# Optimization experiments

Hardware: AMD Instinct MI355X
Metric: run time of the kernel (lower is better)

## Reference

```python
import jax, jax.numpy as jnp
import numpy as np

V = 5000      # vocab_size
N = 10000     # num_training_size
T = 50        # num_topics
H = 200       # en_units
B = 1024      # batch
K = 20        # num_k
ALPHA = 1.0
ETA = 0.5
RHO = 0.5
EPS = 1e-5    # BatchNorm eps
CC = 0.25     # TopicDistQuant commitment cost


def _xavier(key, shape):
    fan_out, fan_in = shape
    lim = float(np.sqrt(6.0 / (fan_in + fan_out)))
    return jax.random.uniform(key, shape, jnp.float32, -lim, lim)


def setup_inputs() -> dict:
    key = jax.random.key(0)
    ks = jax.random.split(key, 10)
    return {
        'idx': jax.random.randint(ks[0], (B,), 0, N),
        'inputs': jax.random.uniform(ks[1], (B, V), jnp.float32),
        'is_aug': 1,
        'training_data': jax.random.uniform(ks[2], (N, V), jnp.float32),
        'M_cos_dist': jax.random.uniform(ks[3], (N, N), jnp.float32),
        'M_coo_dist': jax.random.uniform(ks[4], (N, N), jnp.float32),
        'theta_bank': jax.random.uniform(ks[5], (N, T), jnp.float32),
        'W11': _xavier(ks[6], (H, V)), 'b11': jnp.zeros((H,), jnp.float32),
        'W12': _xavier(ks[7], (H, H)), 'b12': jnp.zeros((H,), jnp.float32),
        'W21': _xavier(ks[8], (T, H)), 'b21': jnp.zeros((T,), jnp.float32),
        'g_mean': jnp.ones((T,), jnp.float32), 'beta_mean': jnp.zeros((T,), jnp.float32),
        'g_dec': jnp.ones((V,), jnp.float32), 'beta_dec': jnp.zeros((V,), jnp.float32),
        'Wd': _xavier(ks[9], (V, T)),
        'E': jnp.eye(T, dtype=jnp.float32),  # TopicDistQuant codebook (identity init)
    }


def _batchnorm(x, g, b):
    # training-mode BatchNorm1d: batch mean, biased variance
    m = x.mean(axis=0)
    v = x.var(axis=0)
    return (x - m) / jnp.sqrt(v + EPS) * g + b


def _forward(idx, inputs, is_aug, training_data, M_cos_dist, M_coo_dist, theta_bank,
             W11, b11, W12, b12, W21, b21, g_mean, beta_mean, g_dec, beta_dec, Wd, E):
    # encoder
    e1 = jax.nn.softplus(inputs @ W11.T + b11)          # [B,H]
    e1 = jax.nn.softplus(e1 @ W12.T + b12)              # [B,H]
    theta = _batchnorm(e1 @ W21.T + b21, g_mean, beta_mean)  # [B,T]
    softmax_theta = jax.nn.softmax(theta, axis=1)

    # TopicDistQuant (VQ with straight-through, identity codebook)
    d = ((softmax_theta ** 2).sum(1, keepdims=True)
         + (E ** 2).sum(1) - 2.0 * softmax_theta @ E.T)  # [B,T]
    enc_idx = jnp.argmin(d, axis=1)                      # [B]
    quantized = E[enc_idx]                               # [B,T]
    e_latent = jnp.mean((jax.lax.stop_gradient(quantized) - softmax_theta) ** 2)
    q_latent = jnp.mean((quantized - jax.lax.stop_gradient(softmax_theta)) ** 2)
    quant_loss = q_latent + CC * e_latent
    quant = softmax_theta + jax.lax.stop_gradient(quantized - softmax_theta)

    # decoder
    recon = jax.nn.softmax(_batchnorm(quant @ Wd.T, g_dec, beta_dec), axis=1)  # [B,V]

    if is_aug:
        # get_aug_x: fused distance + topk + gather-sum over training bank
        td = jax.lax.stop_gradient(softmax_theta)        # theta.detach()
        cost = ((td ** 2).sum(1, keepdims=True)
                + (theta_bank ** 2).sum(1) - 2.0 * td @ theta_bank.T)  # [B,N]
        theta_dist = jnp.square(cost)                    # torch.square(cost)
        bow_dist = RHO * M_cos_dist[idx] + (1.0 - RHO) * M_coo_dist[idx]  # [B,N]
        fuse = ETA * theta_dist + (1.0 - ETA) * bow_dist
        fuse = fuse.at[jnp.arange(B), idx].set(jnp.inf)  # mask self
        _, topk_idx = jax.lax.top_k(-fuse, K)            # K smallest -> [B,K]
        aug_x = (ALPHA / K) * jnp.take(training_data, topk_idx, axis=0).sum(axis=1)  # [B,V]
        x = inputs + aug_x
    else:
        x = inputs

    rec_loss = jnp.mean(-(x * jnp.log(recon)).sum(axis=1))
    return rec_loss + quant_loss


def reference(idx, inputs, is_aug, training_data, M_cos_dist, M_coo_dist, theta_bank,
              W11, b11, W12, b12, W21, b21, g_mean, beta_mean, g_dec, beta_dec, Wd, E):
    return _forward(idx, inputs, is_aug, training_data, M_cos_dist, M_coo_dist, theta_bank,
                    W11, b11, W12, b12, W21, b21, g_mean, beta_mean, g_dec, beta_dec, Wd, E)
```

## Files before the change

kernel.cpp:

```cpp
#include <hip/hip_runtime.h>
#include <math.h>

#define B_ 1024
#define V_ 5000
#define N_ 10000
#define T_ 50
#define H_ 200
#define K_ 20
#define EPS_ 1e-5f

__device__ __forceinline__ float sp_(float x) {
    return (x > 20.f) ? x : log1pf(expf(x));
}

__global__ __launch_bounds__(256) void k_init(float* e1a, float* buckets, int* cnt) {
    int i = blockIdx.x * 256 + threadIdx.x;
    if (i < B_ * H_) e1a[i] = 0.f;
    if (i < 1024)    buckets[i] = 0.f;
    if (i < 64)      cnt[i] = 0;
}

__global__ __launch_bounds__(256) void k_gemm1(const float* __restrict__ X,
                                               const float* __restrict__ W,
                                               float* __restrict__ e1a) {
    __shared__ __align__(16) float Al[64][8];
    __shared__ __align__(16) float Bl[200][8];
    const int tid = threadIdx.x;
    const int r = tid & 31, c = tid >> 5;
    const int m0 = blockIdx.x * 64;
    const int k0 = blockIdx.y * 200;
    float acc0[25], acc1[25];
#pragma unroll
    for (int j = 0; j < 25; ++j) { acc0[j] = 0.f; acc1[j] = 0.f; }
    for (int kb = 0; kb < 200; kb += 8) {
        __syncthreads();
        if (tid < 128) {
            int row = tid >> 1, kp = (tid & 1) * 4;
            *(float4*)&Al[row][kp] = *(const float4*)&X[(size_t)(m0 + row) * V_ + k0 + kb + kp];
        }
        for (int i = tid; i < 400; i += 256) {
            int h = i >> 1, kp = (i & 1) * 4;
            *(float4*)&Bl[h][kp] = *(const float4*)&W[(size_t)h * V_ + k0 + kb + kp];
        }
        __syncthreads();
#pragma unroll
        for (int kc = 0; kc < 8; kc += 4) {
            float4 a0 = *(const float4*)&Al[r][kc];
            float4 a1 = *(const float4*)&Al[r + 32][kc];
#pragma unroll
            for (int j = 0; j < 25; ++j) {
                float4 bb = *(const float4*)&Bl[c * 25 + j][kc];
                acc0[j] += a0.x * bb.x + a0.y * bb.y + a0.z * bb.z + a0.w * bb.w;
                acc1[j] += a1.x * bb.x + a1.y * bb.y + a1.z * bb.z + a1.w * bb.w;
            }
        }
    }
#pragma unroll
    for (int j = 0; j < 25; ++j) {
        atomicAdd(&e1a[(size_t)(m0 + r) * H_ + c * 25 + j], acc0[j]);
        atomicAdd(&e1a[(size_t)(m0 + r + 32) * H_ + c * 25 + j], acc1[j]);
    }
}

__global__ __launch_bounds__(256) void k_enc_tail(const float* __restrict__ e1a,
                                                  const float* __restrict__ b11,
                                                  const float* __restrict__ W12,
                                                  const float* __restrict__ b12,
                                                  const float* __restrict__ W21,
                                                  const float* __restrict__ b21,
                                                  float* __restrict__ thetalin) {
    __shared__ float arow[H_];
    __shared__ float brow[H_];
    __shared__ float Wl[H_ * T_];
    const int b = blockIdx.x, tid = threadIdx.x;
    if (tid < H_) arow[tid] = sp_(e1a[(size_t)b * H_ + tid] + b11[tid]);
    float acc = (tid < H_) ? b12[tid] : 0.f;
    for (int kc = 0; kc < 4; ++kc) {
        __syncthreads();
        for (int i = tid; i < H_ * T_; i += 256) {
            int h = i / T_, k = i % T_;
            Wl[i] = W12[h * H_ + kc * T_ + k];
        }
        __syncthreads();
        if (tid < H_) {
#pragma unroll 10
            for (int k = 0; k < T_; ++k) acc += arow[kc * T_ + k] * Wl[tid * T_ + k];
        }
    }
    __syncthreads();
    if (tid < H_) brow[tid] = sp_(acc);
    __syncthreads();
    for (int i = tid; i < T_ * H_; i += 256) Wl[i] = W21[i];
    __syncthreads();
    if (tid < T_) {
        float a2 = b21[tid];
        for (int h = 0; h < H_; ++h) a2 += brow[h] * Wl[tid * H_ + h];
        thetalin[b * T_ + tid] = a2;
    }
}

__global__ __launch_bounds__(64) void k_bnstats(const float* __restrict__ thetalin,
                                                const float* __restrict__ g,
                                                const float* __restrict__ be,
                                                float* scale, float* shift) {
    int t = threadIdx.x;
    if (t >= T_) return;
    double s = 0.0, s2 = 0.0;
    for (int b = 0; b < B_; ++b) {
        float x = thetalin[b * T_ + t];
        s += x; s2 += (double)x * x;
    }
    double mean = s / B_;
    float var = (float)(s2 / B_ - mean * mean);
    float sc = g[t] / sqrtf(var + EPS_);
    scale[t] = sc;
    shift[t] = be[t] - (float)mean * sc;
}

__global__ __launch_bounds__(64) void k_st(const float* __restrict__ thetalin,
                                           const float* __restrict__ scale,
                                           const float* __restrict__ shift,
                                           float* __restrict__ st, float* __restrict__ stnorm,
                                           int* __restrict__ enc_idx, int* __restrict__ cnt,
                                           float* __restrict__ buckets) {
    const int b = blockIdx.x, t = threadIdx.x;
    float x = (t < T_) ? thetalin[b * T_ + t] * scale[t] + shift[t] : -INFINITY;
    float m = x;
#pragma unroll
    for (int off = 32; off; off >>= 1) m = fmaxf(m, __shfl_xor(m, off));
    float e = (t < T_) ? expf(x - m) : 0.f;
    float ssum = e;
#pragma unroll
    for (int off = 32; off; off >>= 1) ssum += __shfl_xor(ssum, off);
    float stv = e / ssum;
    if (t < T_) st[b * T_ + t] = stv;
    float sn = stv * stv;
#pragma unroll
    for (int off = 32; off; off >>= 1) sn += __shfl_xor(sn, off);
    float bv = x; int bi = (t < T_) ? t : (1 << 30);
#pragma unroll
    for (int off = 32; off; off >>= 1) {
        float ov = __shfl_xor(bv, off); int oi = __shfl_xor(bi, off);
        if (ov > bv || (ov == bv && oi < bi)) { bv = ov; bi = oi; }
    }
    if (t == 0) {
        enc_idx[b] = bi;
        atomicAdd(&cnt[bi], 1);
        stnorm[b] = sn;
        float stmax = 1.f / ssum;
        atomicAdd(&buckets[b], (1.25f / (float)(B_ * T_)) * (sn + 1.f - 2.f * stmax));
    }
}

__global__ __launch_bounds__(256) void k_amat(const float* __restrict__ Wd,
                                              const int* __restrict__ cnt,
                                              const float* __restrict__ gd,
                                              const float* __restrict__ bd,
                                              float* __restrict__ A) {
    __shared__ float cl[T_];
    const int tid = threadIdx.x;
    if (tid < T_) cl[tid] = (float)cnt[tid];
    __syncthreads();
    int v = blockIdx.x * 256 + tid;
    if (v >= V_) return;
    float mean = 0.f, ex2 = 0.f;
#pragma unroll
    for (int t = 0; t < T_; ++t) {
        float w = Wd[v * T_ + t];
        mean += cl[t] * w; ex2 += cl[t] * w * w;
    }
    mean *= (1.f / B_); ex2 *= (1.f / B_);
    float rstd = 1.f / sqrtf(ex2 - mean * mean + EPS_);
    float g = gd[v], bb = bd[v];
#pragma unroll
    for (int t = 0; t < T_; ++t)
        A[(size_t)t * V_ + v] = (Wd[v * T_ + t] - mean) * rstd * g + bb;
}

__global__ __launch_bounds__(256) void k_lse(const float* __restrict__ A, float* __restrict__ lse) {
    __shared__ float red[4];
    const int t = blockIdx.x, tid = threadIdx.x;
    const float* row = A + (size_t)t * V_;
    float m = -INFINITY;
    for (int i = tid; i < V_; i += 256) m = fmaxf(m, row[i]);
#pragma unroll
    for (int off = 32; off; off >>= 1) m = fmaxf(m, __shfl_xor(m, off));
    if ((tid & 63) == 0) red[tid >> 6] = m;
    __syncthreads();
    m = fmaxf(fmaxf(red[0], red[1]), fmaxf(red[2], red[3]));
    float s = 0.f;
    for (int i = tid; i < V_; i += 256) s += expf(row[i] - m);
#pragma unroll
    for (int off = 32; off; off >>= 1) s += __shfl_xor(s, off);
    __syncthreads();
    if ((tid & 63) == 0) red[tid >> 6] = s;
    __syncthreads();
    if (tid == 0) lse[t] = m + logf(red[0] + red[1] + red[2] + red[3]);
}

__global__ __launch_bounds__(256) void k_tbnorm(const float* __restrict__ tb, float* __restrict__ tbn) {
    int n = blockIdx.x * 256 + threadIdx.x;
    if (n >= N_) return;
    float s = 0.f;
#pragma unroll
    for (int t = 0; t < T_; ++t) { float x = tb[n * T_ + t]; s += x * x; }
    tbn[n] = s;
}

__global__ __launch_bounds__(256) void k_fuse_topk(const float* __restrict__ st,
                                                   const float* __restrict__ stnorm,
                                                   const float* __restrict__ tb,
                                                   const float* __restrict__ tbn,
                                                   const float* __restrict__ Mcos,
                                                   const float* __restrict__ Mcoo,
                                                   const int* __restrict__ idx,
                                                   float* __restrict__ cand_v,
                                                   int* __restrict__ cand_i) {
    __shared__ __align__(16) float tbl[256 * T_];
    const int tid = threadIdx.x;
    const int lane = tid & 63, wv = tid >> 6;
    const int half = blockIdx.x & 1;
    const int r = (blockIdx.x >> 1) * 4 + wv;
    const int n0 = half * 5000;
    float sreg[T_];
#pragma unroll
    for (int k = 0; k < T_; ++k) sreg[k] = st[r * T_ + k];
    const float snr = stnorm[r];
    const int myidx = idx[r];
    const float* mcr = Mcos + (size_t)myidx * N_;
    const float* mor = Mcoo + (size_t)myidx * N_;
    float tv[K_]; int ti[K_];
#pragma unroll
    for (int s = 0; s < K_; ++s) { tv[s] = INFINITY; ti[s] = -1; }
    float worst = INFINITY;
    for (int c0 = 0; c0 < 5000; c0 += 256) {
        int nrows = min(256, 5000 - c0);
        __syncthreads();
        {
            const float4* src = (const float4*)(tb + (size_t)(n0 + c0) * T_);
            float4* dst = (float4*)tbl;
            int cnt4 = nrows * T_ / 4;
            for (int i = tid; i < cnt4; i += 256) dst[i] = src[i];
        }
        __syncthreads();
#pragma unroll
        for (int jj = 0; jj < 4; ++jj) {
            int nn = lane + 64 * jj;
            int n = n0 + c0 + nn;
            if (nn < nrows && n != myidx) {
                const float2* t2 = (const float2*)(tbl + nn * T_);
                float d = 0.f;
#pragma unroll
                for (int k = 0; k < T_ / 2; ++k) {
                    float2 w = t2[k];
                    d += sreg[2 * k] * w.x + sreg[2 * k + 1] * w.y;
                }
                float cost = snr + tbn[n] - 2.f * d;
                float f = 0.5f * cost * cost + 0.5f * (0.5f * mcr[n] + 0.5f * mor[n]);
                if (f < worst) {
                    bool done = false;
#pragma unroll
                    for (int s = 0; s < K_; ++s) {
                        bool mm = (!done) && (tv[s] == worst);
                        if (mm) { tv[s] = f; ti[s] = n; done = true; }
                    }
                    worst = tv[0];
#pragma unroll
                    for (int s = 1; s < K_; ++s) worst = fmaxf(worst, tv[s]);
                }
            }
        }
    }
    for (int it = 0; it < K_; ++it) {
        float mv = INFINITY; int mi = -1, ms = -1;
#pragma unroll
        for (int s = 0; s < K_; ++s) {
            bool better = tv[s] < mv;
            mv = better ? tv[s] : mv;
            mi = better ? ti[s] : mi;
            ms = better ? s : ms;
        }
        float bv = mv; int bn = mi, bl = lane, bs = ms;
#pragma unroll
        for (int off = 32; off; off >>= 1) {
            float ov = __shfl_xor(bv, off); int on = __shfl_xor(bn, off);
            int ol = __shfl_xor(bl, off);   int os = __shfl_xor(bs, off);
            if (ov < bv || (ov == bv && on < bn)) { bv = ov; bn = on; bl = ol; bs = os; }
        }
        if (lane == 0) {
            cand_v[(r * 2 + half) * K_ + it] = bv;
            cand_i[(r * 2 + half) * K_ + it] = bn;
        }
        if (lane == bl) {
#pragma unroll
            for (int s = 0; s < K_; ++s)
                if (s == bs) tv[s] = INFINITY;
        }
    }
}

__global__ __launch_bounds__(64) void k_merge40(const float* __restrict__ cand_v,
                                                const int* __restrict__ cand_i,
                                                int* __restrict__ topk) {
    const int b = blockIdx.x, lane = threadIdx.x;
    float v = (lane < 2 * K_) ? cand_v[b * 2 * K_ + lane] : INFINITY;
    int id = (lane < 2 * K_) ? cand_i[b * 2 * K_ + lane] : -1;
    for (int it = 0; it < K_; ++it) {
        float bv = v; int bn = id, bl = lane;
#pragma unroll
        for (int off = 32; off; off >>= 1) {
            float ov = __shfl_xor(bv, off); int on = __shfl_xor(bn, off);
            int ol = __shfl_xor(bl, off);
            if (ov < bv || (ov == bv && on < bn)) { bv = ov; bn = on; bl = ol; }
        }
        if (lane == 0) topk[b * K_ + it] = bn;
        if (lane == bl) v = INFINITY;
    }
}

__global__ __launch_bounds__(256) void k_aug(const float* __restrict__ td,
                                             const float* __restrict__ A,
                                             const float* __restrict__ lse,
                                             const int* __restrict__ topk,
                                             const int* __restrict__ enc_idx,
                                             const int* __restrict__ flag,
                                             float* __restrict__ buckets) {
    __shared__ float red[8];
    const int tid = threadIdx.x;
    const int b = blockIdx.x / K_;
    const int k = blockIdx.x % K_;
    const int j = topk[b * K_ + k];
    const int t = enc_idx[b];
    const float4* trow = (const float4*)(td + (size_t)j * V_);
    const float4* arow = (const float4*)(A + (size_t)t * V_);
    float dot = 0.f, s = 0.f;
    for (int i = tid; i < V_ / 4; i += 256) {
        float4 a = trow[i]; float4 w = arow[i];
        dot += a.x * w.x + a.y * w.y + a.z * w.z + a.w * w.w;
        s += a.x + a.y + a.z + a.w;
    }
#pragma unroll
    for (int off = 32; off; off >>= 1) {
        dot += __shfl_xor(dot, off);
        s += __shfl_xor(s, off);
    }
    if ((tid & 63) == 0) { red[(tid >> 6) * 2] = dot; red[(tid >> 6) * 2 + 1] = s; }
    __syncthreads();
    if (tid == 0 && *flag != 0) {
        float D = red[0] + red[2] + red[4] + red[6];
        float S = red[1] + red[3] + red[5] + red[7];
        atomicAdd(&buckets[blockIdx.x & 1023], (lse[t] * S - D) * (1.f / ((float)B_ * (float)K_)));
    }
}

__global__ __launch_bounds__(256) void k_xin(const float* __restrict__ inputs,
                                             const float* __restrict__ A,
                                             const float* __restrict__ lse,
                                             const int* __restrict__ enc_idx,
                                             float* __restrict__ buckets) {
    __shared__ float red[8];
    const int tid = threadIdx.x, b = blockIdx.x;
    const int t = enc_idx[b];
    const float4* xr = (const float4*)(inputs + (size_t)b * V_);
    const float4* ar = (const float4*)(A + (size_t)t * V_);
    float dot = 0.f, s = 0.f;
    for (int i = tid; i < V_ / 4; i += 256) {
        float4 a = xr[i]; float4 w = ar[i];
        dot += a.x * w.x + a.y * w.y + a.z * w.z + a.w * w.w;
        s += a.x + a.y + a.z + a.w;
    }
#pragma unroll
    for (int off = 32; off; off >>= 1) {
        dot += __shfl_xor(dot, off);
        s += __shfl_xor(s, off);
    }
    if ((tid & 63) == 0) { red[(tid >> 6) * 2] = dot; red[(tid >> 6) * 2 + 1] = s; }
    __syncthreads();
    if (tid == 0) {
        float D = red[0] + red[2] + red[4] + red[6];
        float S = red[1] + red[3] + red[5] + red[7];
        atomicAdd(&buckets[b], (lse[t] * S - D) * (1.f / (float)B_));
    }
}

__global__ __launch_bounds__(256) void k_final(const float* __restrict__ buckets, float* __restrict__ out) {
    __shared__ float red[4];
    const int tid = threadIdx.x;
    float v = buckets[tid] + buckets[tid + 256] + buckets[tid + 512] + buckets[tid + 768];
#pragma unroll
    for (int off = 32; off; off >>= 1) v += __shfl_xor(v, off);
    if ((tid & 63) == 0) red[tid >> 6] = v;
    __syncthreads();
    if (tid == 0) out[0] = red[0] + red[1] + red[2] + red[3];
}

extern "C" void kernel_launch(void* const* d_in, const int* in_sizes, int n_in,
                              void* d_out, int out_size, void* d_ws, size_t ws_size,
                              hipStream_t stream) {
    const int*   idx    = (const int*)d_in[0];
    const float* inputs = (const float*)d_in[1];
    const int*   flag   = (const int*)d_in[2];
    const float* td     = (const float*)d_in[3];
    const float* Mcos   = (const float*)d_in[4];
    const float* Mcoo   = (const float*)d_in[5];
    const float* tb     = (const float*)d_in[6];
    const float* W11    = (const float*)d_in[7];
    const float* b11    = (const float*)d_in[8];
    const float* W12    = (const float*)d_in[9];
    const float* b12    = (const float*)d_in[10];
    const float* W21    = (const float*)d_in[11];
    const float* b21    = (const float*)d_in[12];
    const float* gm     = (const float*)d_in[13];
    const float* bm     = (const float*)d_in[14];
    const float* gd     = (const float*)d_in[15];
    const float* bd     = (const float*)d_in[16];
    const float* Wd     = (const float*)d_in[17];
    float* out = (float*)d_out;

    float* ws       = (float*)d_ws;
    float* e1a      = ws;
    float* thetalin = e1a + 204800;
    float* st       = thetalin + 51200;
    float* stnorm   = st + 51200;
    float* scale    = stnorm + 1024;
    float* shift    = scale + 64;
    float* Amat     = shift + 64;
    float* lse      = Amat + 250000;
    float* tbn      = lse + 64;
    float* buckets  = tbn + 10000;
    float* cand_v   = buckets + 1024;
    int*   enc_idx  = (int*)(cand_v + 40960);
    int*   cnt      = enc_idx + 1024;
    int*   cand_i   = cnt + 64;
    int*   topk     = cand_i + 40960;

    k_init<<<800, 256, 0, stream>>>(e1a, buckets, cnt);
    k_gemm1<<<dim3(16, 25), 256, 0, stream>>>(inputs, W11, e1a);
    k_enc_tail<<<1024, 256, 0, stream>>>(e1a, b11, W12, b12, W21, b21, thetalin);
    k_bnstats<<<1, 64, 0, stream>>>(thetalin, gm, bm, scale, shift);
    k_st<<<1024, 64, 0, stream>>>(thetalin, scale, shift, st, stnorm, enc_idx, cnt, buckets);
    k_amat<<<20, 256, 0, stream>>>(Wd, cnt, gd, bd, Amat);
    k_lse<<<50, 256, 0, stream>>>(Amat, lse);
    k_tbnorm<<<40, 256, 0, stream>>>(tb, tbn);
    k_fuse_topk<<<512, 256, 0, stream>>>(st, stnorm, tb, tbn, Mcos, Mcoo, idx, cand_v, cand_i);
    k_merge40<<<1024, 64, 0, stream>>>(cand_v, cand_i, topk);
    k_aug<<<20480, 256, 0, stream>>>(td, Amat, lse, topk, enc_idx, flag, buckets);
    k_xin<<<1024, 256, 0, stream>>>(inputs, Amat, lse, enc_idx, buckets);
    k_final<<<1, 256, 0, stream>>>(buckets, out);
}
```

Before: 1.379 ms.

## Replace per-neighbor gathered dot products with dense bf16 MFMA over all training rows

The augmentation loss term is now computed by multiplying the entire training_data matrix (N×V) against the decoder log-prob matrix plus a ones row, using bf16 MFMA. A small kernel then looks up the precomputed per-row dot products for each top-k neighbor. This replaces 20480 gathered row-dot blocks, which reread about 400 MB of rows, with one streaming pass over the 200 MB training matrix. The encoder tail is also split into tiled GEMM kernels, and BatchNorm statistics are parallelised per topic. The cost is bf16 rounding in the loss, extra zero-initialised workspace, and atomic accumulation across K-splits.

```diff
diff --git a/kernel.cpp b/kernel.cpp
--- a/kernel.cpp
+++ b/kernel.cpp
@@ -9,112 +9,181 @@
 #define K_ 20
 #define EPS_ 1e-5f
 
+typedef __attribute__((ext_vector_type(8))) short short8_t;
+typedef __attribute__((ext_vector_type(4))) float float4_t;
+
 __device__ __forceinline__ float sp_(float x) {
     return (x > 20.f) ? x : log1pf(expf(x));
 }
 
-__global__ __launch_bounds__(256) void k_init(float* e1a, float* buckets, int* cnt) {
+__device__ __forceinline__ unsigned short f2bf(float x) {
+    union { float f; unsigned int u; } c; c.f = x;
+    unsigned int u = c.u + 0x7fffu + ((c.u >> 16) & 1u);
+    return (unsigned short)(u >> 16);
+}
+
+__global__ __launch_bounds__(256) void k_init(float* e1a, float* e2a, float* Gacc,
+                                              float* buckets, int* cnt) {
     int i = blockIdx.x * 256 + threadIdx.x;
-    if (i < B_ * H_) e1a[i] = 0.f;
-    if (i < 1024)    buckets[i] = 0.f;
-    if (i < 64)      cnt[i] = 0;
+    if (i < 640000)   Gacc[i] = 0.f;
+    if (i < B_ * H_)  { e1a[i] = 0.f; e2a[i] = 0.f; }
+    if (i < 1024)     buckets[i] = 0.f;
+    if (i < 64)       cnt[i] = 0;
 }
 
 __global__ __launch_bounds__(256) void k_gemm1(const float* __restrict__ X,
                                                const float* __restrict__ W,
-                                               float* __restrict__ e1a) {
-    __shared__ __align__(16) float Al[64][8];
-    __shared__ __align__(16) float Bl[200][8];
-    const int tid = threadIdx.x;
-    const int r = tid & 31, c = tid >> 5;
+                                               float* __restrict__ out) {
+    __shared__ __align__(16) float Al[64][28];
+    __shared__ __align__(16) float Bl[200][24];
+    const int tid = threadIdx.x;
+    const int tc = tid & 7, tr = tid >> 3;
     const int m0 = blockIdx.x * 64;
     const int k0 = blockIdx.y * 200;
     float acc0[25], acc1[25];
 #pragma unroll
     for (int j = 0; j < 25; ++j) { acc0[j] = 0.f; acc1[j] = 0.f; }
-    for (int kb = 0; kb < 200; kb += 8) {
-        __syncthreads();
-        if (tid < 128) {
-            int row = tid >> 1, kp = (tid & 1) * 4;
-            *(float4*)&Al[row][kp] = *(const float4*)&X[(size_t)(m0 + row) * V_ + k0 + kb + kp];
-        }
-        for (int i = tid; i < 400; i += 256) {
-            int h = i >> 1, kp = (i & 1) * 4;
-            *(float4*)&Bl[h][kp] = *(const float4*)&W[(size_t)h * V_ + k0 + kb + kp];
-        }
-        __syncthreads();
-#pragma unroll
-        for (int kc = 0; kc < 8; kc += 4) {
-            float4 a0 = *(const float4*)&Al[r][kc];
-            float4 a1 = *(const float4*)&Al[r + 32][kc];
+    for (int kb = 0; kb < 200; kb += 20) {
+        __syncthreads();
+        for (int i = tid; i < 320; i += 256) {
+            int row = i / 5, q = i % 5;
+            *(float4*)&Al[row][q * 4] = *(const float4*)&X[(size_t)(m0 + row) * V_ + k0 + kb + q * 4];
+        }
+        for (int i = tid; i < 1000; i += 256) {
+            int row = i / 5, q = i % 5;
+            *(float4*)&Bl[row][q * 4] = *(const float4*)&W[(size_t)row * V_ + k0 + kb + q * 4];
+        }
+        __syncthreads();
+#pragma unroll
+        for (int kq = 0; kq < 20; kq += 4) {
+            float4 a0 = *(const float4*)&Al[2 * tr][kq];
+            float4 a1 = *(const float4*)&Al[2 * tr + 1][kq];
 #pragma unroll
             for (int j = 0; j < 25; ++j) {
-                float4 bb = *(const float4*)&Bl[c * 25 + j][kc];
-                acc0[j] += a0.x * bb.x + a0.y * bb.y + a0.z * bb.z + a0.w * bb.w;
-                acc1[j] += a1.x * bb.x + a1.y * bb.y + a1.z * bb.z + a1.w * bb.w;
+                float4 b = *(const float4*)&Bl[tc * 25 + j][kq];
+                acc0[j] += a0.x * b.x + a0.y * b.y + a0.z * b.z + a0.w * b.w;
+                acc1[j] += a1.x * b.x + a1.y * b.y + a1.z * b.z + a1.w * b.w;
             }
         }
     }
 #pragma unroll
     for (int j = 0; j < 25; ++j) {
-        atomicAdd(&e1a[(size_t)(m0 + r) * H_ + c * 25 + j], acc0[j]);
-        atomicAdd(&e1a[(size_t)(m0 + r + 32) * H_ + c * 25 + j], acc1[j]);
-    }
-}
-
-__global__ __launch_bounds__(256) void k_enc_tail(const float* __restrict__ e1a,
-                                                  const float* __restrict__ b11,
-                                                  const float* __restrict__ W12,
-                                                  const float* __restrict__ b12,
-                                                  const float* __restrict__ W21,
-                                                  const float* __restrict__ b21,
-                                                  float* __restrict__ thetalin) {
-    __shared__ float arow[H_];
-    __shared__ float brow[H_];
-    __shared__ float Wl[H_ * T_];
-    const int b = blockIdx.x, tid = threadIdx.x;
-    if (tid < H_) arow[tid] = sp_(e1a[(size_t)b * H_ + tid] + b11[tid]);
-    float acc = (tid < H_) ? b12[tid] : 0.f;
-    for (int kc = 0; kc < 4; ++kc) {
-        __syncthreads();
-        for (int i = tid; i < H_ * T_; i += 256) {
-            int h = i / T_, k = i % T_;
-            Wl[i] = W12[h * H_ + kc * T_ + k];
-        }
-        __syncthreads();
-        if (tid < H_) {
-#pragma unroll 10
-            for (int k = 0; k < T_; ++k) acc += arow[kc * T_ + k] * Wl[tid * T_ + k];
-        }
-    }
-    __syncthreads();
-    if (tid < H_) brow[tid] = sp_(acc);
-    __syncthreads();
-    for (int i = tid; i < T_ * H_; i += 256) Wl[i] = W21[i];
-    __syncthreads();
-    if (tid < T_) {
-        float a2 = b21[tid];
-        for (int h = 0; h < H_; ++h) a2 += brow[h] * Wl[tid * H_ + h];
-        thetalin[b * T_ + tid] = a2;
-    }
-}
-
-__global__ __launch_bounds__(64) void k_bnstats(const float* __restrict__ thetalin,
-                                                const float* __restrict__ g,
-                                                const float* __restrict__ be,
-                                                float* scale, float* shift) {
-    int t = threadIdx.x;
-    if (t >= T_) return;
-    double s = 0.0, s2 = 0.0;
-    for (int b = 0; b < B_; ++b) {
-        float x = thetalin[b * T_ + t];
-        s += x; s2 += (double)x * x;
-    }
-    double mean = s / B_;
-    float var = (float)(s2 / B_ - mean * mean);
-    float sc = g[t] / sqrtf(var + EPS_);
-    scale[t] = sc;
-    shift[t] = be[t] - (float)mean * sc;
+        atomicAdd(&out[(size_t)(m0 + 2 * tr) * H_ + tc * 25 + j], acc0[j]);
+        atomicAdd(&out[(size_t)(m0 + 2 * tr + 1) * H_ + tc * 25 + j], acc1[j]);
+    }
+}
+
+__global__ __launch_bounds__(256) void k_sp(const float* __restrict__ acc,
+                                            const float* __restrict__ bias,
+                                            float* __restrict__ out) {
+    int i = blockIdx.x * 256 + threadIdx.x;
+    if (i < B_ * H_) out[i] = sp_(acc[i] + bias[i % H_]);
+}
+
+__global__ __launch_bounds__(256) void k_gemm2(const float* __restrict__ X,
+                                               const float* __restrict__ W,
+                                               float* __restrict__ out) {
+    __shared__ __align__(16) float Al[64][28];
+    __shared__ __align__(16) float Bl[200][24];
+    const int tid = threadIdx.x;
+    const int tc = tid & 7, tr = tid >> 3;
+    const int m0 = blockIdx.x * 64;
+    const int k0 = blockIdx.y * 100;
+    float acc0[25], acc1[25];
+#pragma unroll
+    for (int j = 0; j < 25; ++j) { acc0[j] = 0.f; acc1[j] = 0.f; }
+    for (int kb = 0; kb < 100; kb += 20) {
+        __syncthreads();
+        for (int i = tid; i < 320; i += 256) {
+            int row = i / 5, q = i % 5;
+            *(float4*)&Al[row][q * 4] = *(const float4*)&X[(size_t)(m0 + row) * H_ + k0 + kb + q * 4];
+        }
+        for (int i = tid; i < 1000; i += 256) {
+            int row = i / 5, q = i % 5;
+            *(float4*)&Bl[row][q * 4] = *(const float4*)&W[(size_t)row * H_ + k0 + kb + q * 4];
+        }
+        __syncthreads();
+#pragma unroll
+        for (int kq = 0; kq < 20; kq += 4) {
+            float4 a0 = *(const float4*)&Al[2 * tr][kq];
+            float4 a1 = *(const float4*)&Al[2 * tr + 1][kq];
+#pragma unroll
+            for (int j = 0; j < 25; ++j) {
+                float4 b = *(const float4*)&Bl[tc * 25 + j][kq];
+                acc0[j] += a0.x * b.x + a0.y * b.y + a0.z * b.z + a0.w * b.w;
+                acc1[j] += a1.x * b.x + a1.y * b.y + a1.z * b.z + a1.w * b.w;
+            }
+        }
+    }
+#pragma unroll
+    for (int j = 0; j < 25; ++j) {
+        atomicAdd(&out[(size_t)(m0 + 2 * tr) * H_ + tc * 25 + j], acc0[j]);
+        atomicAdd(&out[(size_t)(m0 + 2 * tr + 1) * H_ + tc * 25 + j], acc1[j]);
+    }
+}
+
+__global__ __launch_bounds__(128) void k_gemm3(const float* __restrict__ X,
+                                               const float* __restrict__ W,
+                                               const float* __restrict__ bias,
+                                               float* __restrict__ out) {
+    __shared__ __align__(16) float Al[64][28];
+    __shared__ __align__(16) float Bl[50][24];
+    const int tid = threadIdx.x;
+    const int tc = tid & 1, tr = tid >> 1;
+    const int m0 = blockIdx.x * 64;
+    float acc[25];
+#pragma unroll
+    for (int j = 0; j < 25; ++j) acc[j] = 0.f;
+    for (int kb = 0; kb < 200; kb += 20) {
+        __syncthreads();
+        for (int i = tid; i < 320; i += 128) {
+            int row = i / 5, q = i % 5;
+            *(float4*)&Al[row][q * 4] = *(const float4*)&X[(size_t)(m0 + row) * H_ + kb + q * 4];
+        }
+        for (int i = tid; i < 250; i += 128) {
+            int row = i / 5, q = i % 5;
+            *(float4*)&Bl[row][q * 4] = *(const float4*)&W[(size_t)row * H_ + kb + q * 4];
+        }
+        __syncthreads();
+#pragma unroll
+        for (int kq = 0; kq < 20; kq += 4) {
+            float4 a0 = *(const float4*)&Al[tr][kq];
+#pragma unroll
+            for (int j = 0; j < 25; ++j) {
+                float4 b = *(const float4*)&Bl[tc * 25 + j][kq];
+                acc[j] += a0.x * b.x + a0.y * b.y + a0.z * b.z + a0.w * b.w;
+            }
+        }
+    }
+#pragma unroll
+    for (int j = 0; j < 25; ++j)
+        out[(size_t)(m0 + tr) * T_ + tc * 25 + j] = acc[j] + bias[tc * 25 + j];
+}
+
+__global__ __launch_bounds__(256) void k_bnstats(const float* __restrict__ th,
+                                                 const float* __restrict__ g,
+                                                 const float* __restrict__ be,
+                                                 float* scale, float* shift) {
+    __shared__ float r1[4], r2[4];
+    const int t = blockIdx.x, tid = threadIdx.x;
+    float s = 0.f, s2 = 0.f;
+    for (int b = tid; b < B_; b += 256) {
+        float x = th[b * T_ + t];
+        s += x; s2 += x * x;
+    }
+#pragma unroll
+    for (int off = 32; off; off >>= 1) { s += __shfl_xor(s, off); s2 += __shfl_xor(s2, off); }
+    if ((tid & 63) == 0) { r1[tid >> 6] = s; r2[tid >> 6] = s2; }
+    __syncthreads();
+    if (tid == 0) {
+        float S = r1[0] + r1[1] + r1[2] + r1[3];
+        float S2 = r2[0] + r2[1] + r2[2] + r2[3];
+        float mean = S * (1.f / B_);
+        float var = S2 * (1.f / B_) - mean * mean;
+        float sc = g[t] / sqrtf(var + EPS_);
+        scale[t] = sc;
+        shift[t] = be[t] - mean * sc;
+    }
 }
 
 __global__ __launch_bounds__(64) void k_st(const float* __restrict__ thetalin,
@@ -156,7 +225,8 @@
                                               const int* __restrict__ cnt,
                                               const float* __restrict__ gd,
                                               const float* __restrict__ bd,
-                                              float* __restrict__ A) {
+                                              float* __restrict__ A,
+                                              unsigned short* __restrict__ Bbf) {
     __shared__ float cl[T_];
     const int tid = threadIdx.x;
     if (tid < T_) cl[tid] = (float)cnt[tid];
@@ -173,8 +243,14 @@
     float rstd = 1.f / sqrtf(ex2 - mean * mean + EPS_);
     float g = gd[v], bb = bd[v];
 #pragma unroll
-    for (int t = 0; t < T_; ++t)
-        A[(size_t)t * V_ + v] = (Wd[v * T_ + t] - mean) * rstd * g + bb;
+    for (int t = 0; t < T_; ++t) {
+        float val = (Wd[v * T_ + t] - mean) * rstd * g + bb;
+        A[(size_t)t * V_ + v] = val;
+        Bbf[(size_t)t * V_ + v] = f2bf(val);
+    }
+    Bbf[(size_t)50 * V_ + v] = 0x3F80u;
+#pragma unroll
+    for (int r = 51; r < 64; ++r) Bbf[(size_t)r * V_ + v] = 0u;
 }
 
 __global__ __launch_bounds__(256) void k_lse(const float* __restrict__ A, float* __restrict__ lse) {
@@ -318,39 +394,85 @@
     }
 }
 
-__global__ __launch_bounds__(256) void k_aug(const float* __restrict__ td,
-                                             const float* __restrict__ A,
-                                             const float* __restrict__ lse,
-                                             const int* __restrict__ topk,
-                                             const int* __restrict__ enc_idx,
-                                             const int* __restrict__ flag,
-                                             float* __restrict__ buckets) {
-    __shared__ float red[8];
-    const int tid = threadIdx.x;
-    const int b = blockIdx.x / K_;
-    const int k = blockIdx.x % K_;
-    const int j = topk[b * K_ + k];
+__global__ __launch_bounds__(256) void k_gmm(const float* __restrict__ td,
+                                             const unsigned short* __restrict__ Bbf,
+                                             float* __restrict__ Gacc) {
+    __shared__ __align__(16) unsigned short At[128][40];
+    __shared__ __align__(16) unsigned short Bt[64][40];
+    const int tid = threadIdx.x;
+    const int lane = tid & 63, w = tid >> 6;
+    const int lm = lane & 15, kg = lane >> 4;
+    const int m0 = blockIdx.x * 128;
+    const int ks = blockIdx.y * 1280;
+    float4_t acc[8];
+#pragma unroll
+    for (int mt = 0; mt < 8; ++mt)
+#pragma unroll
+        for (int r = 0; r < 4; ++r) acc[mt][r] = 0.f;
+
+    const int arow = tid >> 1, ahf = tid & 1;
+    const int brow = tid >> 2, bq = tid & 3;
+
+    for (int ch = 0; ch < 40; ++ch) {
+        const int kk = ks + ch * 32;
+        __syncthreads();
+        {
+            const size_t base = (size_t)(m0 + arow) * V_ + kk + ahf * 16;
+            unsigned int p[8];
+            bool rok = (m0 + arow) < N_;
+#pragma unroll
+            for (int q = 0; q < 4; ++q) {
+                float4 x = (rok && (kk + ahf * 16 + q * 4) < V_)
+                           ? *(const float4*)&td[base + q * 4]
+                           : make_float4(0.f, 0.f, 0.f, 0.f);
+                p[q * 2]     = (unsigned int)f2bf(x.x) | ((unsigned int)f2bf(x.y) << 16);
+                p[q * 2 + 1] = (unsigned int)f2bf(x.z) | ((unsigned int)f2bf(x.w) << 16);
+            }
+            *(uint4*)&At[arow][ahf * 16]     = *(uint4*)&p[0];
+            *(uint4*)&At[arow][ahf * 16 + 8] = *(uint4*)&p[4];
+        }
+        {
+            uint4 bv = make_uint4(0, 0, 0, 0);
+            if ((kk + bq * 8) < V_)
+                bv = *(const uint4*)&Bbf[(size_t)brow * V_ + kk + bq * 8];
+            *(uint4*)&Bt[brow][bq * 8] = bv;
+        }
+        __syncthreads();
+        short8_t bfrag = *(const short8_t*)&Bt[16 * w + lm][kg * 8];
+#pragma unroll
+        for (int mt = 0; mt < 8; ++mt) {
+            short8_t afrag = *(const short8_t*)&At[16 * mt + lm][kg * 8];
+            acc[mt] = __builtin_amdgcn_mfma_f32_16x16x32_bf16(afrag, bfrag, acc[mt], 0, 0, 0);
+        }
+    }
+    const int col = 16 * w + lm;
+#pragma unroll
+    for (int mt = 0; mt < 8; ++mt) {
+#pragma unroll
+        for (int r = 0; r < 4; ++r) {
+            int row = m0 + 16 * mt + kg * 4 + r;
+            if (row < N_) atomicAdd(&Gacc[(size_t)row * 64 + col], acc[mt][r]);
+        }
+    }
+}
+
+__global__ __launch_bounds__(64) void k_augnew(const float* __restrict__ Gacc,
+                                               const float* __restrict__ lse,
+                                               const int* __restrict__ topk,
+                                               const int* __restrict__ enc_idx,
+                                               const int* __restrict__ flag,
+                                               float* __restrict__ buckets) {
+    const int b = blockIdx.x, l = threadIdx.x;
     const int t = enc_idx[b];
-    const float4* trow = (const float4*)(td + (size_t)j * V_);
-    const float4* arow = (const float4*)(A + (size_t)t * V_);
-    float dot = 0.f, s = 0.f;
-    for (int i = tid; i < V_ / 4; i += 256) {
-        float4 a = trow[i]; float4 w = arow[i];
-        dot += a.x * w.x + a.y * w.y + a.z * w.z + a.w * w.w;
-        s += a.x + a.y + a.z + a.w;
-    }
-#pragma unroll
-    for (int off = 32; off; off >>= 1) {
-        dot += __shfl_xor(dot, off);
-        s += __shfl_xor(s, off);
-    }
-    if ((tid & 63) == 0) { red[(tid >> 6) * 2] = dot; red[(tid >> 6) * 2 + 1] = s; }
-    __syncthreads();
-    if (tid == 0 && *flag != 0) {
-        float D = red[0] + red[2] + red[4] + red[6];
-        float S = red[1] + red[3] + red[5] + red[7];
-        atomicAdd(&buckets[blockIdx.x & 1023], (lse[t] * S - D) * (1.f / ((float)B_ * (float)K_)));
-    }
+    float v = 0.f;
+    if (l < K_) {
+        int j = topk[b * K_ + l];
+        v = lse[t] * Gacc[(size_t)j * 64 + 50] - Gacc[(size_t)j * 64 + t];
+    }
+#pragma unroll
+    for (int off = 32; off; off >>= 1) v += __shfl_xor(v, off);
+    if (l == 0 && *flag != 0)
+        atomicAdd(&buckets[b], v * (1.f / ((float)B_ * (float)K_)));
 }
 
 __global__ __launch_bounds__(256) void k_xin(const float* __restrict__ inputs,
@@ -365,8 +487,8 @@
     const float4* ar = (const float4*)(A + (size_t)t * V_);
     float dot = 0.f, s = 0.f;
     for (int i = tid; i < V_ / 4; i += 256) {
-        float4 a = xr[i]; float4 w = ar[i];
-        dot += a.x * w.x + a.y * w.y + a.z * w.z + a.w * w.w;
+        float4 a = xr[i]; float4 wv = ar[i];
+        dot += a.x * wv.x + a.y * wv.y + a.z * wv.z + a.w * wv.w;
         s += a.x + a.y + a.z + a.w;
     }
 #pragma unroll
@@ -419,7 +541,10 @@
 
     float* ws       = (float*)d_ws;
     float* e1a      = ws;
-    float* thetalin = e1a + 204800;
+    float* e1       = e1a + 204800;
+    float* e2a      = e1 + 204800;
+    float* e2       = e2a + 204800;
+    float* thetalin = e2 + 204800;
     float* st       = thetalin + 51200;
     float* stnorm   = st + 51200;
     float* scale    = stnorm + 1024;
@@ -429,22 +554,28 @@
     float* tbn      = lse + 64;
     float* buckets  = tbn + 10000;
     float* cand_v   = buckets + 1024;
-    int*   enc_idx  = (int*)(cand_v + 40960);
+    float* Gacc     = cand_v + 40960;
+    unsigned short* Bbf = (unsigned short*)(Gacc + 640000);
+    int*   enc_idx  = (int*)(Gacc + 640000 + 160000);
     int*   cnt      = enc_idx + 1024;
     int*   cand_i   = cnt + 64;
     int*   topk     = cand_i + 40960;
 
-    k_init<<<800, 256, 0, stream>>>(e1a, buckets, cnt);
+    k_init<<<2500, 256, 0, stream>>>(e1a, e2a, Gacc, buckets, cnt);
     k_gemm1<<<dim3(16, 25), 256, 0, stream>>>(inputs, W11, e1a);
-    k_enc_tail<<<1024, 256, 0, stream>>>(e1a, b11, W12, b12, W21, b21, thetalin);
-    k_bnstats<<<1, 64, 0, stream>>>(thetalin, gm, bm, scale, shift);
+    k_sp<<<800, 256, 0, stream>>>(e1a, b11, e1);
+    k_gemm2<<<dim3(16, 2), 256, 0, stream>>>(e1, W12, e2a);
+    k_sp<<<800, 256, 0, stream>>>(e2a, b12, e2);
+    k_gemm3<<<16, 128, 0, stream>>>(e2, W21, b21, thetalin);
+    k_bnstats<<<50, 256, 0, stream>>>(thetalin, gm, bm, scale, shift);
     k_st<<<1024, 64, 0, stream>>>(thetalin, scale, shift, st, stnorm, enc_idx, cnt, buckets);
-    k_amat<<<20, 256, 0, stream>>>(Wd, cnt, gd, bd, Amat);
+    k_amat<<<20, 256, 0, stream>>>(Wd, cnt, gd, bd, Amat, Bbf);
     k_lse<<<50, 256, 0, stream>>>(Amat, lse);
     k_tbnorm<<<40, 256, 0, stream>>>(tb, tbn);
     k_fuse_topk<<<512, 256, 0, stream>>>(st, stnorm, tb, tbn, Mcos, Mcoo, idx, cand_v, cand_i);
     k_merge40<<<1024, 64, 0, stream>>>(cand_v, cand_i, topk);
-    k_aug<<<20480, 256, 0, stream>>>(td, Amat, lse, topk, enc_idx, flag, buckets);
+    k_gmm<<<dim3(79, 4), 256, 0, stream>>>(td, Bbf, Gacc);
+    k_augnew<<<1024, 64, 0, stream>>>(Gacc, lse, topk, enc_idx, flag, buckets);
     k_xin<<<1024, 256, 0, stream>>>(inputs, Amat, lse, enc_idx, buckets);
     k_final<<<1, 256, 0, stream>>>(buckets, out);
 }
```

After: 1.537 ms. 11.4% more time.
